# Kernel tuning notes

Measured on AMD Instinct MI355X. Metric: run time of the kernel, lower is better.

The kernel has to match this reference:

```python
import jax, jax.numpy as jnp
import numpy as np

N = 25000   # nodes
M = 150000  # edges
D = 512     # d_Embedding
H = 8       # heads
DK = 64     # per-head key dim
DV = 64     # per-head value dim


def setup_inputs() -> dict:
    key = jax.random.key(0)
    ks = jax.random.split(key, 8)
    x = jax.random.normal(ks[0], (N, D), jnp.float32)
    edge_index = jax.random.randint(ks[1], (2, M), 0, N).astype(jnp.int32)
    s_in = 1.0 / np.sqrt(D).astype(np.float32)   # fan-in scaling like nn.Linear init
    s_ff = 1.0 / np.sqrt(H * DV).astype(np.float32)
    Wk = jax.random.normal(ks[2], (D, H * DK), jnp.float32) * s_in
    Wq = jax.random.normal(ks[3], (D, H * DK), jnp.float32) * s_in
    Wv = jax.random.normal(ks[4], (D, H * DV), jnp.float32) * s_in
    Wff = jax.random.normal(ks[5], (H * DV, D), jnp.float32) * s_ff
    bk = jnp.zeros((H * DK,), jnp.float32)
    bq = jnp.zeros((H * DK,), jnp.float32)
    bv = jnp.zeros((H * DV,), jnp.float32)
    bff = jnp.zeros((D,), jnp.float32)
    return {"x": x, "edge_index": edge_index, "Wk": Wk, "bk": bk,
            "Wq": Wq, "bq": bq, "Wv": Wv, "bv": bv, "Wff": Wff, "bff": bff}


def reference(x, edge_index, Wk, bk, Wq, bq, Wv, bv, Wff, bff):
    # Q/K/V projections with per-head reshape (make_heads)
    K = (x @ Wk + bk).reshape(-1, H, DK)
    Q = (x @ Wq + bq).reshape(-1, H, DK)
    V = (x @ Wv + bv).reshape(-1, H, DV)
    senders, receivers = edge_index[0], edge_index[1]
    # edge scores: (M, H)
    att = jnp.einsum('mhd,mhd->mh', Q[receivers], K[senders]) / np.sqrt(DK).astype(np.float32)
    att = jnp.exp(att + 3.0 - att.max())  # global-max-shifted exp, as in source
    # normalize by sum of incoming strengths per receiver node (segment softmax denom)
    ssum = jax.ops.segment_sum(att, receivers, num_segments=N)  # (N, H)
    denom = ssum[receivers]
    att = jnp.where(denom == 0, 0.0, att / jnp.where(denom == 0, 1.0, denom))
    # weighted message + scatter-add aggregate: (N, H, DV)
    msg = att[..., None] * V[senders]
    agg = jax.ops.segment_sum(msg, receivers, num_segments=N)
    # aggregate_heads: Linear over concatenated heads
    return agg.reshape(-1, H * DV) @ Wff + bff
```

## Files before the change

kernel.cpp:

```cpp
#include <hip/hip_runtime.h>
#include <hip/hip_bf16.h>

#define DMODEL 512

typedef __attribute__((ext_vector_type(8))) short bf16x8;
typedef __attribute__((ext_vector_type(4))) float f32x4;

__device__ inline void gload_lds16(const void* g, void* s) {
  __builtin_amdgcn_global_load_lds((const __attribute__((address_space(1))) void*)g,
                                   (__attribute__((address_space(3))) void*)s, 16, 0, 0);
}

__device__ inline float bflo(unsigned u) {
  union { float f; unsigned u; } c; c.u = u << 16; return c.f;
}
__device__ inline float bfhi(unsigned u) {
  union { float f; unsigned u; } c; c.u = u & 0xffff0000u; return c.f;
}

template <bool OUT_BF16>
__global__ __launch_bounds__(512, 2)
void gemm_stripe(const __hip_bfloat16* __restrict__ Ap,
                 const __hip_bfloat16* __restrict__ Wp,
                 const float* __restrict__ bias, void* __restrict__ Cv,
                 int Nrows, int ncols, int nquads, int G) {
  __shared__ __align__(16) short sB[32768];
  const int tid = threadIdx.x;
  const int lane = tid & 63, w = tid >> 6;
  const int g = blockIdx.x, stripe = blockIdx.y;
  const int col0 = stripe * 64;
  const __hip_bfloat16* Ws = Wp + (size_t)stripe * 32768;

#pragma unroll
  for (int i = 0; i < 8; ++i)
    gload_lds16(Ws + (size_t)(i * 512 + tid) * 8, &sB[(i * 512 + tid) * 8]);
  __syncthreads();

  const int l15 = lane & 15, lq = lane >> 4;

  for (int q = g * 8 + w; q < nquads; q += G * 8) {
    f32x4 acc[4][4] = {};
    const __hip_bfloat16* Abase = Ap + (size_t)q * 32768 + lane * 8;
    bf16x8 a_cur[4], a_nxt[4];
#pragma unroll
    for (int m = 0; m < 4; ++m)
      a_cur[m] = *(const bf16x8*)(Abase + m * 8192);

#pragma unroll 1
    for (int c = 0; c < 16; ++c) {
      if (c < 15) {
#pragma unroll
        for (int m = 0; m < 4; ++m)
          a_nxt[m] = *(const bf16x8*)(Abase + m * 8192 + (c + 1) * 512);
      }
#pragma unroll
      for (int n = 0; n < 4; ++n) {
        bf16x8 bf = *(const bf16x8*)&sB[((n * 16 + c) * 64 + lane) * 8];
#pragma unroll
        for (int m = 0; m < 4; ++m)
          acc[m][n] = __builtin_amdgcn_mfma_f32_16x16x32_bf16(a_cur[m], bf, acc[m][n], 0, 0, 0);
      }
      if (c < 15) {
#pragma unroll
        for (int m = 0; m < 4; ++m) a_cur[m] = a_nxt[m];
      }
    }

#pragma unroll
    for (int m = 0; m < 4; ++m) {
      int rowb = q * 64 + m * 16;
#pragma unroll
      for (int n = 0; n < 4; ++n) {
        int col = col0 + n * 16 + l15;
        float bv = bias[col];
#pragma unroll
        for (int i = 0; i < 4; ++i) {
          int row = rowb + lq * 4 + i;
          if (row < Nrows) {
            float v = acc[m][n][i] + bv;
            if (OUT_BF16)
              ((__hip_bfloat16*)Cv)[(size_t)row * ncols + col] = __float2bfloat16(v);
            else
              ((float*)Cv)[(size_t)row * ncols + col] = v;
          }
        }
      }
    }
  }
}

__global__ void cvtp_kernel(const float* __restrict__ x, __hip_bfloat16* __restrict__ xp,
                            int Nrows, int NpadRows) {
  int tid = blockIdx.x * 256 + threadIdx.x;
  int r = tid >> 6, kb = tid & 63;
  if (r >= NpadRows) return;
  int t = r >> 4, c = kb >> 2, qq = kb & 3, lp = qq * 16 + (r & 15);
  __hip_bfloat16* dst = xp + (size_t)t * 8192 + c * 512 + lp * 8;
  union { ushort4 u[2]; __hip_bfloat16 h[8]; } o;
#pragma unroll
  for (int j = 0; j < 8; ++j) o.h[j] = __float2bfloat16(0.f);
  if (r < Nrows) {
    float4 v0 = *(const float4*)(x + (size_t)r * DMODEL + kb * 8);
    float4 v1 = *(const float4*)(x + (size_t)r * DMODEL + kb * 8 + 4);
    o.h[0] = __float2bfloat16(v0.x); o.h[1] = __float2bfloat16(v0.y);
    o.h[2] = __float2bfloat16(v0.z); o.h[3] = __float2bfloat16(v0.w);
    o.h[4] = __float2bfloat16(v1.x); o.h[5] = __float2bfloat16(v1.y);
    o.h[6] = __float2bfloat16(v1.z); o.h[7] = __float2bfloat16(v1.w);
  }
  *(ushort4*)dst = o.u[0];
  *(ushort4*)(dst + 4) = o.u[1];
}

__global__ __launch_bounds__(256)
void wp_kernel(const float* __restrict__ Wk, const float* __restrict__ Wq,
               const float* __restrict__ Wv, const float* __restrict__ Wff,
               __hip_bfloat16* __restrict__ Wp_qkv, __hip_bfloat16* __restrict__ Wp_ff) {
  int c = blockIdx.x;
  int S = blockIdx.y;
  const float* W; __hip_bfloat16* dst;
  if (S < 8)       { W = Wk;  dst = Wp_qkv + (size_t)S * 32768; }
  else if (S < 16) { W = Wq;  dst = Wp_qkv + (size_t)S * 32768; }
  else if (S < 24) { W = Wv;  dst = Wp_qkv + (size_t)S * 32768; }
  else             { W = Wff; dst = Wp_ff + (size_t)(S - 24) * 32768; }
  int colbase = (S & 7) * 64;
  __shared__ float tile[32][64];
  for (int idx = threadIdx.x; idx < 2048; idx += 256) {
    int r = idx >> 6, col = idx & 63;
    tile[r][col] = W[(size_t)(c * 32 + r) * DMODEL + colbase + col];
  }
  __syncthreads();
  int n = threadIdx.x >> 6, l = threadIdx.x & 63;
  union { ushort4 u[2]; __hip_bfloat16 h[8]; } o;
#pragma unroll
  for (int j = 0; j < 8; ++j)
    o.h[j] = __float2bfloat16(tile[(l >> 4) * 8 + j][n * 16 + (l & 15)]);
  __hip_bfloat16* p = dst + ((size_t)(n * 16 + c) * 64 + l) * 8;
  *(ushort4*)p = o.u[0];
  *(ushort4*)(p + 4) = o.u[1];
}

__global__ void bias_kernel(const float* __restrict__ bk, const float* __restrict__ bq,
                            const float* __restrict__ bv, float* __restrict__ o) {
  int i = blockIdx.x * 256 + threadIdx.x;
  if (i < 512) o[i] = bk[i];
  else if (i < 1024) o[i] = bq[i - 512];
  else if (i < 1536) o[i] = bv[i - 1024];
}

__global__ void hist_kernel(const int* __restrict__ recv, int* __restrict__ deg, int M_) {
  int m = blockIdx.x * 256 + threadIdx.x;
  if (m < M_) atomicAdd(&deg[recv[m]], 1);
}

__global__ __launch_bounds__(256)
void scan_block(const int* __restrict__ deg, int* __restrict__ offs,
                int* __restrict__ bsum, int n) {
  __shared__ int sd[256];
  const int t = threadIdx.x;
  const int base = blockIdx.x * 1024;
  int v[4], s = 0;
#pragma unroll
  for (int j = 0; j < 4; ++j) {
    int idx = base + t * 4 + j;
    v[j] = (idx < n) ? deg[idx] : 0;
    s += v[j];
  }
  sd[t] = s;
  __syncthreads();
  for (int off = 1; off < 256; off <<= 1) {
    int x = (t >= off) ? sd[t - off] : 0;
    __syncthreads();
    sd[t] += x;
    __syncthreads();
  }
  int run = sd[t] - s;
#pragma unroll
  for (int j = 0; j < 4; ++j) {
    int idx = base + t * 4 + j;
    if (idx < n) offs[idx] = run;
    run += v[j];
  }
  if (t == 255) bsum[blockIdx.x] = sd[255];
}

__global__ void scan_mid(const int* __restrict__ bsum, int* __restrict__ bbase,
                         int nb, int* __restrict__ offs, int n) {
  int t = threadIdx.x;
  int x = (t < nb) ? bsum[t] : 0;
  int v = x;
  for (int off = 1; off < 64; off <<= 1) {
    int y = __shfl_up(v, off);
    if (t >= off) v += y;
  }
  if (t < nb) bbase[t] = v - x;
  if (t == nb - 1) offs[n] = v;
}

__global__ void scan_add(int* __restrict__ offs, const int* __restrict__ bbase,
                         int* __restrict__ cursor, int n) {
  int i = blockIdx.x * 256 + threadIdx.x;
  if (i < n) {
    int o = offs[i] + bbase[i >> 10];
    offs[i] = o;
    cursor[i] = o;
  }
}

__global__ void fill_kernel(const int* __restrict__ senders, const int* __restrict__ recv,
                            int* __restrict__ cursor, int* __restrict__ sidx, int M_) {
  int m = blockIdx.x * 256 + threadIdx.x;
  if (m < M_) {
    int pos = atomicAdd(&cursor[recv[m]], 1);
    sidx[pos] = senders[m];
  }
}

__global__ __launch_bounds__(256)
void attn_kernel(const __hip_bfloat16* __restrict__ QKV, const int* __restrict__ sidx,
                 const int* __restrict__ offs, __hip_bfloat16* __restrict__ aggp, int n) {
  const int lane = threadIdx.x & 63;
  const int wid  = threadIdx.x >> 6;
  const int r = blockIdx.x * 4 + wid;
  if (r >= n) return;
  const int start = offs[r];
  const int end   = offs[r + 1];

  uint4 qr = *(const uint4*)(QKV + (size_t)r * 1536 + 512 + lane * 8);
  float q[8] = {bflo(qr.x), bfhi(qr.x), bflo(qr.y), bfhi(qr.y),
                bflo(qr.z), bfhi(qr.z), bflo(qr.w), bfhi(qr.w)};

  float ssum = 0.f;
  float acc[8] = {};
  int e = start;
  for (; e + 2 <= end; e += 2) {
    int s0 = sidx[e], s1 = sidx[e + 1];
    const __hip_bfloat16* p0 = QKV + (size_t)s0 * 1536 + lane * 8;
    const __hip_bfloat16* p1 = QKV + (size_t)s1 * 1536 + lane * 8;
    uint4 k0 = *(const uint4*)p0;
    uint4 v0 = *(const uint4*)(p0 + 1024);
    uint4 k1 = *(const uint4*)p1;
    uint4 v1 = *(const uint4*)(p1 + 1024);
    float d0 = q[0] * bflo(k0.x) + q[1] * bfhi(k0.x) + q[2] * bflo(k0.y) + q[3] * bfhi(k0.y)
             + q[4] * bflo(k0.z) + q[5] * bfhi(k0.z) + q[6] * bflo(k0.w) + q[7] * bfhi(k0.w);
    float d1 = q[0] * bflo(k1.x) + q[1] * bfhi(k1.x) + q[2] * bflo(k1.y) + q[3] * bfhi(k1.y)
             + q[4] * bflo(k1.z) + q[5] * bfhi(k1.z) + q[6] * bflo(k1.w) + q[7] * bfhi(k1.w);
    d0 += __shfl_xor(d0, 1); d1 += __shfl_xor(d1, 1);
    d0 += __shfl_xor(d0, 2); d1 += __shfl_xor(d1, 2);
    d0 += __shfl_xor(d0, 4); d1 += __shfl_xor(d1, 4);
    float w0 = expf(d0 * 0.125f), w1 = expf(d1 * 0.125f);
    ssum += w0 + w1;
    acc[0] += w0 * bflo(v0.x) + w1 * bflo(v1.x);
    acc[1] += w0 * bfhi(v0.x) + w1 * bfhi(v1.x);
    acc[2] += w0 * bflo(v0.y) + w1 * bflo(v1.y);
    acc[3] += w0 * bfhi(v0.y) + w1 * bfhi(v1.y);
    acc[4] += w0 * bflo(v0.z) + w1 * bflo(v1.z);
    acc[5] += w0 * bfhi(v0.z) + w1 * bfhi(v1.z);
    acc[6] += w0 * bflo(v0.w) + w1 * bflo(v1.w);
    acc[7] += w0 * bfhi(v0.w) + w1 * bfhi(v1.w);
  }
  if (e < end) {
    int s0 = sidx[e];
    const __hip_bfloat16* p0 = QKV + (size_t)s0 * 1536 + lane * 8;
    uint4 k0 = *(const uint4*)p0;
    uint4 v0 = *(const uint4*)(p0 + 1024);
    float d0 = q[0] * bflo(k0.x) + q[1] * bfhi(k0.x) + q[2] * bflo(k0.y) + q[3] * bfhi(k0.y)
             + q[4] * bflo(k0.z) + q[5] * bfhi(k0.z) + q[6] * bflo(k0.w) + q[7] * bfhi(k0.w);
    d0 += __shfl_xor(d0, 1);
    d0 += __shfl_xor(d0, 2);
    d0 += __shfl_xor(d0, 4);
    float w0 = expf(d0 * 0.125f);
    ssum += w0;
    acc[0] += w0 * bflo(v0.x); acc[1] += w0 * bfhi(v0.x);
    acc[2] += w0 * bflo(v0.y); acc[3] += w0 * bfhi(v0.y);
    acc[4] += w0 * bflo(v0.z); acc[5] += w0 * bfhi(v0.z);
    acc[6] += w0 * bflo(v0.w); acc[7] += w0 * bfhi(v0.w);
  }
  const float inv = (end > start) ? 1.0f / ssum : 0.f;
  union { ushort4 u[2]; __hip_bfloat16 h[8]; } o;
#pragma unroll
  for (int j = 0; j < 8; ++j) o.h[j] = __float2bfloat16(acc[j] * inv);
  int t = r >> 4, c = lane >> 2, qq = lane & 3, lp = qq * 16 + (r & 15);
  __hip_bfloat16* dst = aggp + (size_t)t * 8192 + c * 512 + lp * 8;
  *(ushort4*)dst = o.u[0];
  *(ushort4*)(dst + 4) = o.u[1];
}

extern "C" void kernel_launch(void* const* d_in, const int* in_sizes, int n_in,
                              void* d_out, int out_size, void* d_ws, size_t ws_size,
                              hipStream_t stream) {
  const float* x    = (const float*)d_in[0];
  const int*   eidx = (const int*)d_in[1];
  const float* Wk   = (const float*)d_in[2];
  const float* bk   = (const float*)d_in[3];
  const float* Wq   = (const float*)d_in[4];
  const float* bq   = (const float*)d_in[5];
  const float* Wv   = (const float*)d_in[6];
  const float* bv   = (const float*)d_in[7];
  const float* Wff  = (const float*)d_in[8];
  const float* bff  = (const float*)d_in[9];
  float* out = (float*)d_out;

  const int N_ = in_sizes[0] / DMODEL;
  const int M_ = in_sizes[1] / 2;
  const int* senders = eidx;
  const int* recv    = eidx + M_;

  const int T16 = (N_ + 15) / 16;
  const int Q4  = (T16 + 3) / 4;
  const int Npad = Q4 * 64;

  __hip_bfloat16* xp    = (__hip_bfloat16*)d_ws;
  __hip_bfloat16* QKVb  = xp + (size_t)Npad * DMODEL;
  __hip_bfloat16* aggp  = QKVb + (size_t)N_ * 1536;
  __hip_bfloat16* Wp_qkv = aggp + (size_t)Npad * DMODEL;
  __hip_bfloat16* Wp_ff  = Wp_qkv + (size_t)24 * 32768;
  float* bqkv = (float*)(Wp_ff + (size_t)8 * 32768);
  int* deg    = (int*)(bqkv + 1536);
  int* offs   = deg + N_;
  int* cursor = offs + N_ + 1;
  int* sidx   = cursor + N_;
  int* bsum   = sidx + M_;
  int* bbase  = bsum + 64;

  const int nblk = (N_ + 1023) / 1024;

  cvtp_kernel<<<(Npad * 64 + 255) / 256, 256, 0, stream>>>(x, xp, N_, Npad);
  wp_kernel<<<dim3(16, 32), 256, 0, stream>>>(Wk, Wq, Wv, Wff, Wp_qkv, Wp_ff);
  bias_kernel<<<6, 256, 0, stream>>>(bk, bq, bv, bqkv);

  hipMemsetAsync(deg, 0, N_ * sizeof(int), stream);
  hist_kernel<<<(M_ + 255) / 256, 256, 0, stream>>>(recv, deg, M_);
  scan_block<<<nblk, 256, 0, stream>>>(deg, offs, bsum, N_);
  scan_mid<<<1, 64, 0, stream>>>(bsum, bbase, nblk, offs, N_);
  scan_add<<<(N_ + 255) / 256, 256, 0, stream>>>(offs, bbase, cursor, N_);
  fill_kernel<<<(M_ + 255) / 256, 256, 0, stream>>>(senders, recv, cursor, sidx, M_);

  const int Gq = 21;
  gemm_stripe<true><<<dim3(Gq, 24), 512, 0, stream>>>(xp, Wp_qkv, bqkv, QKVb,
                                                      N_, 1536, Q4, Gq);

  attn_kernel<<<(N_ + 3) / 4, 256, 0, stream>>>(QKVb, sidx, offs, aggp, N_);

  const int Go = 63;
  gemm_stripe<false><<<dim3(Go, 8), 512, 0, stream>>>(aggp, Wp_ff, bff, out,
                                                      N_, DMODEL, Q4, Go);
}
```

Before: 333.7 us.

## Stage activation row-quads in LDS and stream weights from global

Swaps the GEMM's operand roles. Each block now owns one 64-row activation quad, staged in LDS, and its waves walk over column tiles whose weights are streamed from global memory with register prefetch. The earlier version kept a 64-column weight stripe resident in LDS and persistently iterated over row quads. The goal is to read each activation row once per block and drop the persistent grid-stride loop. In exchange, weights are re-read from global (L2) by every block, and the grid becomes one block per quad.

```diff
diff --git a/kernel.cpp b/kernel.cpp
--- a/kernel.cpp
+++ b/kernel.cpp
@@ -18,51 +18,52 @@
   union { float f; unsigned u; } c; c.u = u & 0xffff0000u; return c.f;
 }
 
-template <bool OUT_BF16>
+template <bool OUT_BF16, int NT>
 __global__ __launch_bounds__(512, 2)
-void gemm_stripe(const __hip_bfloat16* __restrict__ Ap,
-                 const __hip_bfloat16* __restrict__ Wp,
-                 const float* __restrict__ bias, void* __restrict__ Cv,
-                 int Nrows, int ncols, int nquads, int G) {
-  __shared__ __align__(16) short sB[32768];
+void gemm_quad(const __hip_bfloat16* __restrict__ Ap,
+               const __hip_bfloat16* __restrict__ Wp,
+               const float* __restrict__ bias, void* __restrict__ Cv,
+               int Nrows, int ncols) {
+  __shared__ __align__(16) short sA[32768];
   const int tid = threadIdx.x;
   const int lane = tid & 63, w = tid >> 6;
-  const int g = blockIdx.x, stripe = blockIdx.y;
-  const int col0 = stripe * 64;
-  const __hip_bfloat16* Ws = Wp + (size_t)stripe * 32768;
+  const int q = blockIdx.x;
+  const __hip_bfloat16* Aq = Ap + (size_t)q * 32768;
 
 #pragma unroll
   for (int i = 0; i < 8; ++i)
-    gload_lds16(Ws + (size_t)(i * 512 + tid) * 8, &sB[(i * 512 + tid) * 8]);
+    gload_lds16(Aq + (size_t)(i * 512 + tid) * 8, &sA[(i * 512 + tid) * 8]);
   __syncthreads();
 
   const int l15 = lane & 15, lq = lane >> 4;
 
-  for (int q = g * 8 + w; q < nquads; q += G * 8) {
+#pragma unroll 1
+  for (int gs = 0; gs < NT / 4; ++gs) {
+    const int ntb = w * NT + gs * 4;
+    const __hip_bfloat16* Wb = Wp + (size_t)ntb * 16 * 512 + lane * 8;
     f32x4 acc[4][4] = {};
-    const __hip_bfloat16* Abase = Ap + (size_t)q * 32768 + lane * 8;
-    bf16x8 a_cur[4], a_nxt[4];
-#pragma unroll
-    for (int m = 0; m < 4; ++m)
-      a_cur[m] = *(const bf16x8*)(Abase + m * 8192);
+    bf16x8 b_cur[4], b_nxt[4];
+#pragma unroll
+    for (int n = 0; n < 4; ++n)
+      b_cur[n] = *(const bf16x8*)(Wb + (size_t)(n * 16) * 512);
 
 #pragma unroll 1
     for (int c = 0; c < 16; ++c) {
       if (c < 15) {
 #pragma unroll
-        for (int m = 0; m < 4; ++m)
-          a_nxt[m] = *(const bf16x8*)(Abase + m * 8192 + (c + 1) * 512);
+        for (int n = 0; n < 4; ++n)
+          b_nxt[n] = *(const bf16x8*)(Wb + (size_t)(n * 16 + c + 1) * 512);
       }
 #pragma unroll
-      for (int n = 0; n < 4; ++n) {
-        bf16x8 bf = *(const bf16x8*)&sB[((n * 16 + c) * 64 + lane) * 8];
-#pragma unroll
-        for (int m = 0; m < 4; ++m)
-          acc[m][n] = __builtin_amdgcn_mfma_f32_16x16x32_bf16(a_cur[m], bf, acc[m][n], 0, 0, 0);
+      for (int m = 0; m < 4; ++m) {
+        bf16x8 af = *(const bf16x8*)&sA[(m * 16 + c) * 512 + lane * 8];
+#pragma unroll
+        for (int n = 0; n < 4; ++n)
+          acc[m][n] = __builtin_amdgcn_mfma_f32_16x16x32_bf16(af, b_cur[n], acc[m][n], 0, 0, 0);
       }
       if (c < 15) {
 #pragma unroll
-        for (int m = 0; m < 4; ++m) a_cur[m] = a_nxt[m];
+        for (int n = 0; n < 4; ++n) b_cur[n] = b_nxt[n];
       }
     }
 
@@ -71,7 +72,7 @@
       int rowb = q * 64 + m * 16;
 #pragma unroll
       for (int n = 0; n < 4; ++n) {
-        int col = col0 + n * 16 + l15;
+        int col = (ntb + n) * 16 + l15;
         float bv = bias[col];
 #pragma unroll
         for (int i = 0; i < 4; ++i) {
@@ -335,13 +336,9 @@
   scan_add<<<(N_ + 255) / 256, 256, 0, stream>>>(offs, bbase, cursor, N_);
   fill_kernel<<<(M_ + 255) / 256, 256, 0, stream>>>(senders, recv, cursor, sidx, M_);
 
-  const int Gq = 21;
-  gemm_stripe<true><<<dim3(Gq, 24), 512, 0, stream>>>(xp, Wp_qkv, bqkv, QKVb,
-                                                      N_, 1536, Q4, Gq);
+  gemm_quad<true, 12><<<Q4, 512, 0, stream>>>(xp, Wp_qkv, bqkv, QKVb, N_, 1536);
 
   attn_kernel<<<(N_ + 3) / 4, 256, 0, stream>>>(QKVb, sidx, offs, aggp, N_);
 
-  const int Go = 63;
-  gemm_stripe<false><<<dim3(Go, 8), 512, 0, stream>>>(aggp, Wp_ff, bff, out,
-                                                      N_, DMODEL, Q4, Go);
-}
+  gemm_quad<false, 4><<<Q4, 512, 0, stream>>>(aggp, Wp_ff, bff, out, N_, DMODEL);
+}
```

Result: faster. 311.5 us (-6.7%).
